# Kernel optimization log

Measured on AMD Instinct MI355X. Metric: run time of the kernel, lower is better.

Reference implementation:

```python
import jax, jax.numpy as jnp
import numpy as np

B, S, D_MODEL, D_QK = 4, 4096, 256, 64


def setup_inputs() -> dict:
    key = jax.random.key(0)
    ks = jax.random.split(key, 6)
    enc_q = jax.random.normal(ks[0], (B, S, D_MODEL), dtype=jnp.float32)
    enc_k = jax.random.normal(ks[1], (B, S, D_MODEL), dtype=jnp.float32)
    enc_v = jax.random.normal(ks[2], (B, S, D_MODEL), dtype=jnp.float32)
    # torch nn.Linear weight layout: [out_features, in_features]
    Wq = jax.random.normal(ks[3], (D_QK, D_MODEL), dtype=jnp.float32) * (D_MODEL ** -0.5)
    Wk = jax.random.normal(ks[4], (D_QK, D_MODEL), dtype=jnp.float32) * (D_MODEL ** -0.5)
    Wv = jax.random.normal(ks[5], (D_MODEL, D_MODEL), dtype=jnp.float32) * (D_MODEL ** -0.5)
    # causal mask: True above the diagonal -> masked out (matches masked_fill semantics)
    mask = jnp.triu(jnp.ones((S, S), dtype=jnp.bool_), k=1)
    return {"encodings_for_q": enc_q, "encodings_for_k": enc_k,
            "encodings_for_v": enc_v, "mask": mask,
            "Wq": Wq, "Wk": Wk, "Wv": Wv}


def reference(encodings_for_q, encodings_for_k, encodings_for_v, mask, Wq, Wk, Wv):
    # linear projections (no bias): x @ W.T
    q = jnp.einsum('bsd,qd->bsq', encodings_for_q, Wq)   # [B,S,d_qk]
    k = jnp.einsum('bsd,qd->bsq', encodings_for_k, Wk)   # [B,S,d_qk]
    v = jnp.einsum('bsd,ed->bse', encodings_for_v, Wv)   # [B,S,d_model]
    scale = k.shape[-1] ** 0.5                            # sqrt(d_qk)
    sims = jnp.einsum('bsq,btq->bst', q, k) / scale       # [B,S,S]
    sims = jnp.where(mask, jnp.float32(-1e9), sims)
    attn = jax.nn.softmax(sims, axis=-1)
    return jnp.einsum('bst,bte->bse', attn, v)            # [B,S,d_model]
```

## Files before the change

### kernel.cpp

```cpp
#include <hip/hip_runtime.h>


#define BATCH 4
#define SEQ   4096
#define DM    256
#define DQK   64

typedef __bf16 bf16x8 __attribute__((ext_vector_type(8)));
typedef __bf16 bf16x2 __attribute__((ext_vector_type(2)));
typedef float  f32x16 __attribute__((ext_vector_type(16)));

__device__ __forceinline__ unsigned short f2bf(float f) {
    __bf16 h = (__bf16)f;
    return __builtin_bit_cast(unsigned short, h);
}
__device__ __forceinline__ unsigned int pk2bf(float lo, float hi) {
    bf16x2 v = {(__bf16)lo, (__bf16)hi};
    return __builtin_bit_cast(unsigned int, v);
}
__device__ __forceinline__ bf16x8 u4bf(uint4 u) { return __builtin_bit_cast(bf16x8, u); }

__device__ __forceinline__ void repack_store(const f32x16& acc, int q2, int l,
                                             uint4* __restrict__ out, size_t tile_ofs_u4) {
    unsigned int d0[4], d1[4], p0[4], p1[4];
#pragma unroll
    for (int h = 0; h < 4; ++h) {
        d0[h] = pk2bf(acc[4*h + 0], acc[4*h + 1]);
        d1[h] = pk2bf(acc[4*h + 2], acc[4*h + 3]);
        p0[h] = __shfl_xor((int)d0[h], 32);
        p1[h] = __shfl_xor((int)d1[h], 32);
    }
#pragma unroll
    for (int kc = 0; kc < 2; ++kc) {
        int h = 2*kc + q2;
        uint4 v = (q2 == 0) ? make_uint4(d0[h], d1[h], p0[h], p1[h])
                            : make_uint4(p0[h], p1[h], d0[h], d1[h]);
        out[tile_ofs_u4 + (size_t)kc * 64 + l] = v;
    }
}

__device__ __forceinline__ int obase(int T) {
    return (T < 24) ? (T - 12) : 12 + (T - 24) * 2;
}
__device__ __forceinline__ int dbase(int T) {
    return (T < 24) ? (T - 12) * 2 : 24 + (T - 24) * 3;
}

__global__ __launch_bounds__(256) void proj(const float* __restrict__ Xq,
                                            const float* __restrict__ Xk,
                                            const float* __restrict__ Xv,
                                            const float* __restrict__ Wq,
                                            const float* __restrict__ Wk,
                                            const float* __restrict__ Wv,
                                            uint4* __restrict__ qf,
                                            uint4* __restrict__ kf,
                                            uint4* __restrict__ vf) {
    __shared__ unsigned short Xs[64][264];
    __shared__ unsigned short Ws[64][264];

    const int z = blockIdx.z;
    const int bx = blockIdx.x, b = blockIdx.y;
    const float* X = (z == 0) ? Xq : (z == 1) ? Xk : Xv;
    const float* W = (z == 0) ? Wq : (z == 1) ? Wk : Wv;
    const int s0 = bx * 64;
    const int tid = threadIdx.x, w = tid >> 6, l = tid & 63, ln = l & 31, q2 = l >> 5;

#pragma unroll
    for (int i = 0; i < 16; ++i) {
        int f = i * 256 + tid;
        int r = f >> 6, c4 = f & 63;
        float4 xv = *(const float4*)&X[((size_t)b * SEQ + s0 + r) * DM + c4 * 4];
        ushort4 h; h.x = f2bf(xv.x); h.y = f2bf(xv.y); h.z = f2bf(xv.z); h.w = f2bf(xv.w);
        *(ushort4*)&Xs[r][c4 * 4] = h;
    }

    if (z < 2) {
#pragma unroll
        for (int i = 0; i < 16; ++i) {
            int f = i * 256 + tid;
            int r = f >> 6, c4 = f & 63;
            float4 wv = *(const float4*)&W[(size_t)r * DM + c4 * 4];
            ushort4 h; h.x = f2bf(wv.x); h.y = f2bf(wv.y); h.z = f2bf(wv.z); h.w = f2bf(wv.w);
            *(ushort4*)&Ws[r][c4 * 4] = h;
        }
        __syncthreads();
        const int msub = w >> 1, nsub = w & 1;
        f32x16 a0 = {}, a1 = {};
#pragma unroll
        for (int c = 0; c < 16; c += 2) {
            bf16x8 af0 = u4bf(*(const uint4*)&Ws[msub*32 + ln][c*16 + q2*8]);
            bf16x8 bf0 = u4bf(*(const uint4*)&Xs[nsub*32 + ln][c*16 + q2*8]);
            a0 = __builtin_amdgcn_mfma_f32_32x32x16_bf16(af0, bf0, a0, 0, 0, 0);
            bf16x8 af1 = u4bf(*(const uint4*)&Ws[msub*32 + ln][(c+1)*16 + q2*8]);
            bf16x8 bf1 = u4bf(*(const uint4*)&Xs[nsub*32 + ln][(c+1)*16 + q2*8]);
            a1 = __builtin_amdgcn_mfma_f32_32x32x16_bf16(af1, bf1, a1, 0, 0, 0);
        }
        f32x16 acc = a0 + a1;
        size_t base = (((size_t)(b*128 + bx*2 + nsub)) * 4 + 2*msub) * 64;
        repack_store(acc, q2, l, (z == 0) ? qf : kf, base);
    } else {
        const int msub = w & 1, nsub = w >> 1;
        for (int ec = 0; ec < 4; ++ec) {
            __syncthreads();
#pragma unroll
            for (int i = 0; i < 16; ++i) {
                int f = i * 256 + tid;
                int r = f >> 6, c4 = f & 63;
                float4 wv = *(const float4*)&W[(size_t)(ec*64 + r) * DM + c4 * 4];
                ushort4 h; h.x = f2bf(wv.x); h.y = f2bf(wv.y); h.z = f2bf(wv.z); h.w = f2bf(wv.w);
                *(ushort4*)&Ws[r][c4 * 4] = h;
            }
            __syncthreads();
            f32x16 a0 = {}, a1 = {};
#pragma unroll
            for (int c = 0; c < 16; c += 2) {
                bf16x8 af0 = u4bf(*(const uint4*)&Xs[msub*32 + ln][c*16 + q2*8]);
                bf16x8 bf0 = u4bf(*(const uint4*)&Ws[nsub*32 + ln][c*16 + q2*8]);
                a0 = __builtin_amdgcn_mfma_f32_32x32x16_bf16(af0, bf0, a0, 0, 0, 0);
                bf16x8 af1 = u4bf(*(const uint4*)&Xs[msub*32 + ln][(c+1)*16 + q2*8]);
                bf16x8 bf1 = u4bf(*(const uint4*)&Ws[nsub*32 + ln][(c+1)*16 + q2*8]);
                a1 = __builtin_amdgcn_mfma_f32_32x32x16_bf16(af1, bf1, a1, 0, 0, 0);
            }
            f32x16 acc = a0 + a1;
            int et = ec*2 + nsub;
            size_t base = (((size_t)(b*8 + et)) * 256 + (size_t)bx*4 + msub*2) * 64;
            repack_store(acc, q2, l, vf, base);
        }
    }
}

__global__ __launch_bounds__(512, 2) void attn(const uint4* __restrict__ qf,
                                               const uint4* __restrict__ kf,
                                               const uint4* __restrict__ vf,
                                               float* __restrict__ out,
                                               unsigned short* __restrict__ Op,
                                               float* __restrict__ Dp) {
    __shared__ uint4 Pb[2][2][8][64];
    __shared__ float denp[4][2][64];
    __shared__ float dfin[64];

    const int bid = blockIdx.x;
    const int slot = bid & 7;
    const int b = slot >> 1, qh = slot & 1;
    const int task = bid >> 3;
    int T, cc, nc;
    if (task < 12)      { T = task;                cc = 0;               nc = 1; }
    else if (task < 36) { int q = task - 12; T = 12 + (q >> 1); cc = q & 1;       nc = 2; }
    else                { int q = task - 36; T = 24 + q / 3;    cc = q - 3*(q/3); nc = 3; }
    const int n = T + 1;
    const int j0 = cc * n / nc, j1 = (cc + 1) * n / nc;

    const int tid = threadIdx.x, w = tid >> 6, l = tid & 63, ln = l & 31, q2 = l >> 5;
    const int ks = w & 3, qg = w >> 2;
    const int qsub = qh * 2 + qg;
    const int et = w;
    const float cfac = 0.18033688011112042f;

    bf16x8 qv[4];
#pragma unroll
    for (int c = 0; c < 4; ++c)
        qv[c] = u4bf(qf[(((size_t)b*128 + T*4 + qsub) * 4 + c) * 64 + l]);

    f32x16 oa[2] = {};
    float den = 0.f;

    uint4 kaf[4];
#pragma unroll
    for (int c = 0; c < 4; ++c)
        kaf[c] = kf[(((size_t)b*128 + j0*4 + ks) * 4 + c) * 64 + l];

    for (int jt = j0; jt < j1; ++jt) {
        const int buf = jt & 1;
        const bool diag = (jt == T);

        uint4 vbs[8];
#pragma unroll
        for (int kc = 0; kc < 8; ++kc)
            vbs[kc] = vf[(((size_t)b*8 + et) * 256 + (size_t)jt*8 + kc) * 64 + l];

        f32x16 s = {};
#pragma unroll
        for (int c = 0; c < 4; ++c)
            s = __builtin_amdgcn_mfma_f32_32x32x16_bf16(u4bf(kaf[c]), qv[c], s, 0, 0, 0);

        float pv[16], pd = 0.f;
#pragma unroll
        for (int r = 0; r < 16; ++r) {
            float e = __builtin_exp2f(s[r] * cfac);
            if (diag) {
                int klocal = 4*q2 + (r & 3) + 8*(r >> 2);
                if (ks*32 + klocal > qsub*32 + ln) e = 0.f;
            }
            pv[r] = e; pd += e;
        }
        den += pd;
#pragma unroll
        for (int quad = 0; quad < 4; ++quad) {
            unsigned int lo = pk2bf(pv[4*quad + 0], pv[4*quad + 1]);
            unsigned int hi = pk2bf(pv[4*quad + 2], pv[4*quad + 3]);
            int kcg = ks*2 + (quad >> 1);
            int h   = quad & 1;
            char* dst = (char*)&Pb[buf][qg][kcg][h*32 + ln] + q2*8;
            *(uint2*)dst = make_uint2(lo, hi);
        }
        __syncthreads();
        if (jt + 1 < j1) {
#pragma unroll
            for (int c = 0; c < 4; ++c)
                kaf[c] = kf[(((size_t)b*128 + (jt+1)*4 + ks) * 4 + c) * 64 + l];
        }
#pragma unroll
        for (int kc = 0; kc < 8; ++kc) {
            bf16x8 vb = u4bf(vbs[kc]);
#pragma unroll
            for (int qsl = 0; qsl < 2; ++qsl) {
                bf16x8 pa = u4bf(Pb[buf][qsl][kc][l]);
                oa[qsl] = __builtin_amdgcn_mfma_f32_32x32x16_bf16(pa, vb, oa[qsl], 0, 0, 0);
            }
        }
    }

    denp[ks][qg][l] = den;
    __syncthreads();
    if (tid < 64) {
        int qgl = tid >> 5, qln = tid & 31;
        float sden = 0.f;
#pragma unroll
        for (int p = 0; p < 4; ++p)
#pragma unroll
            for (int hh = 0; hh < 2; ++hh)
                sden += denp[p][qgl][hh*32 + qln];
        dfin[tid] = (nc == 1) ? 1.0f / sden : sden;
    }
    __syncthreads();

    if (nc == 1) {
#pragma unroll
        for (int qsl = 0; qsl < 2; ++qsl)
#pragma unroll
            for (int r = 0; r < 16; ++r) {
                int qrow = qsl*32 + (r & 3) + 8*(r >> 2) + 4*q2;
                out[((size_t)b*SEQ + T*128 + qh*64 + qrow) * DM + et*32 + ln] = oa[qsl][r] * dfin[qrow];
            }
    } else if (cc == 0) {
#pragma unroll
        for (int qsl = 0; qsl < 2; ++qsl)
#pragma unroll
            for (int r = 0; r < 16; ++r) {
                int qrow = qsl*32 + (r & 3) + 8*(r >> 2) + 4*q2;
                out[((size_t)b*SEQ + T*128 + qh*64 + qrow) * DM + et*32 + ln] = oa[qsl][r];
            }
        if (tid < 64) Dp[((size_t)b*48 + dbase(T)) * 128 + qh*64 + tid] = dfin[tid];
    } else {
        size_t pidx = (size_t)b*28 + obase(T) + (cc - 1);
#pragma unroll
        for (int qsl = 0; qsl < 2; ++qsl)
#pragma unroll
            for (int r = 0; r < 16; ++r) {
                int qrow = qsl*32 + (r & 3) + 8*(r >> 2) + 4*q2;
                Op[(pidx*128 + qh*64 + qrow) * DM + et*32 + ln] = f2bf(oa[qsl][r]);
            }
        if (tid < 64) Dp[((size_t)b*48 + dbase(T) + cc) * 128 + qh*64 + tid] = dfin[tid];
    }
}

__global__ __launch_bounds__(256) void combine(const unsigned short* __restrict__ Op,
                                               const float* __restrict__ Dp,
                                               float* __restrict__ out) {
    const int T = 12 + blockIdx.x, b = blockIdx.y, qq = blockIdx.z;
    const int nc = (T < 24) ? 2 : 3;
    const int t = threadIdx.x;
    const size_t db = (size_t)b*48 + dbase(T);
    const size_t pb = (size_t)b*28 + obase(T);
#pragma unroll 4
    for (int r = 0; r < 32; ++r) {
        int q = qq*32 + r;
        size_t oofs = ((size_t)b*SEQ + T*128 + q) * DM + t;
        float sum = out[oofs];
        float dsum = 0.f;
        for (int c = 0; c < nc; ++c) dsum += Dp[(db + c)*128 + q];
        for (int c = 1; c < nc; ++c) {
            unsigned int uv = Op[((pb + c - 1)*128 + q) * DM + t];
            sum += __builtin_bit_cast(float, uv << 16);
        }
        out[oofs] = sum / dsum;
    }
}

extern "C" void kernel_launch(void* const* d_in, const int* in_sizes, int n_in,
                              void* d_out, int out_size, void* d_ws, size_t ws_size,
                              hipStream_t stream) {
    const float* enc_q = (const float*)d_in[0];
    const float* enc_k = (const float*)d_in[1];
    const float* enc_v = (const float*)d_in[2];
    const float* Wq = (const float*)d_in[4];
    const float* Wk = (const float*)d_in[5];
    const float* Wv = (const float*)d_in[6];
    float* out = (float*)d_out;

    uint4* qf = (uint4*)d_ws;
    uint4* kf = qf + 131072;
    uint4* vf = kf + 131072;
    unsigned short* Op = (unsigned short*)(vf + 524288);
    float* Dp = (float*)(Op + (size_t)4*28*128*256);

    proj<<<dim3(64, 4, 3), 256, 0, stream>>>(enc_q, enc_k, enc_v, Wq, Wk, Wv, qf, kf, vf);
    attn<<<480, 512, 0, stream>>>(qf, kf, vf, out, Op, Dp);
    combine<<<dim3(20, 4, 4), 256, 0, stream>>>(Op, Dp, out);
}
```

Measured before the change: 203.9 us.

## Split attention blocks over output halves, keep P in registers via lane shuffles

The attention kernel now launches twice as many 256-thread blocks, each handling half of the value/output columns, with every wave owning a 32-key slice for both query sub-tiles. P is passed to the PV MFMA through cross-lane shuffles instead of LDS, which removes the per-iteration __syncthreads. Partial outputs from the four key-slice waves are reduced through LDS at the end and written as vectorised stores. The trade is that QK^T and exp are recomputed by both output-half blocks, and the epilogue reduction adds extra LDS traffic and higher register pressure.

```diff
diff --git a/kernel.cpp b/kernel.cpp
--- a/kernel.cpp
+++ b/kernel.cpp
@@ -129,20 +129,21 @@
     }
 }
 
-__global__ __launch_bounds__(512, 2) void attn(const uint4* __restrict__ qf,
+__global__ __launch_bounds__(256, 2) void attn(const uint4* __restrict__ qf,
                                                const uint4* __restrict__ kf,
                                                const uint4* __restrict__ vf,
                                                float* __restrict__ out,
                                                unsigned short* __restrict__ Op,
                                                float* __restrict__ Dp) {
-    __shared__ uint4 Pb[2][2][8][64];
+    __shared__ float Lep[4][2][2][32][36];
     __shared__ float denp[4][2][64];
     __shared__ float dfin[64];
 
     const int bid = blockIdx.x;
     const int slot = bid & 7;
     const int b = slot >> 1, qh = slot & 1;
-    const int task = bid >> 3;
+    const int te = bid >> 3;
+    const int task = te >> 1, eh = te & 1;
     int T, cc, nc;
     if (task < 12)      { T = task;                cc = 0;               nc = 1; }
     else if (task < 36) { int q = task - 12; T = 12 + (q >> 1); cc = q & 1;       nc = 2; }
@@ -151,116 +152,152 @@
     const int j0 = cc * n / nc, j1 = (cc + 1) * n / nc;
 
     const int tid = threadIdx.x, w = tid >> 6, l = tid & 63, ln = l & 31, q2 = l >> 5;
-    const int ks = w & 3, qg = w >> 2;
-    const int qsub = qh * 2 + qg;
-    const int et = w;
+    const int ks = w;
     const float cfac = 0.18033688011112042f;
 
-    bf16x8 qv[4];
-#pragma unroll
-    for (int c = 0; c < 4; ++c)
-        qv[c] = u4bf(qf[(((size_t)b*128 + T*4 + qsub) * 4 + c) * 64 + l]);
-
-    f32x16 oa[2] = {};
-    float den = 0.f;
+    bf16x8 qv[2][4];
+#pragma unroll
+    for (int qs = 0; qs < 2; ++qs)
+#pragma unroll
+        for (int c = 0; c < 4; ++c)
+            qv[qs][c] = u4bf(qf[(((size_t)b*128 + T*4 + qh*2 + qs) * 4 + c) * 64 + l]);
 
     uint4 kaf[4];
 #pragma unroll
     for (int c = 0; c < 4; ++c)
         kaf[c] = kf[(((size_t)b*128 + j0*4 + ks) * 4 + c) * 64 + l];
 
+    f32x16 oa[2][4] = {};
+    float den[2] = {0.f, 0.f};
+
     for (int jt = j0; jt < j1; ++jt) {
-        const int buf = jt & 1;
         const bool diag = (jt == T);
 
-        uint4 vbs[8];
-#pragma unroll
-        for (int kc = 0; kc < 8; ++kc)
-            vbs[kc] = vf[(((size_t)b*8 + et) * 256 + (size_t)jt*8 + kc) * 64 + l];
-
-        f32x16 s = {};
-#pragma unroll
-        for (int c = 0; c < 4; ++c)
-            s = __builtin_amdgcn_mfma_f32_32x32x16_bf16(u4bf(kaf[c]), qv[c], s, 0, 0, 0);
-
-        float pv[16], pd = 0.f;
-#pragma unroll
-        for (int r = 0; r < 16; ++r) {
-            float e = __builtin_exp2f(s[r] * cfac);
-            if (diag) {
-                int klocal = 4*q2 + (r & 3) + 8*(r >> 2);
-                if (ks*32 + klocal > qsub*32 + ln) e = 0.f;
-            }
-            pv[r] = e; pd += e;
-        }
-        den += pd;
-#pragma unroll
-        for (int quad = 0; quad < 4; ++quad) {
-            unsigned int lo = pk2bf(pv[4*quad + 0], pv[4*quad + 1]);
-            unsigned int hi = pk2bf(pv[4*quad + 2], pv[4*quad + 3]);
-            int kcg = ks*2 + (quad >> 1);
-            int h   = quad & 1;
-            char* dst = (char*)&Pb[buf][qg][kcg][h*32 + ln] + q2*8;
-            *(uint2*)dst = make_uint2(lo, hi);
-        }
-        __syncthreads();
+        uint4 vbs[4][2];
+#pragma unroll
+        for (int e4 = 0; e4 < 4; ++e4)
+#pragma unroll
+            for (int t = 0; t < 2; ++t)
+                vbs[e4][t] = vf[(((size_t)b*8 + eh*4 + e4) * 256 + (size_t)jt*8 + ks*2 + t) * 64 + l];
+
+        f32x16 s0 = {}, s1 = {};
+#pragma unroll
+        for (int c = 0; c < 4; ++c) {
+            bf16x8 ka = u4bf(kaf[c]);
+            s0 = __builtin_amdgcn_mfma_f32_32x32x16_bf16(ka, qv[0][c], s0, 0, 0, 0);
+            s1 = __builtin_amdgcn_mfma_f32_32x32x16_bf16(ka, qv[1][c], s1, 0, 0, 0);
+        }
         if (jt + 1 < j1) {
 #pragma unroll
             for (int c = 0; c < 4; ++c)
                 kaf[c] = kf[(((size_t)b*128 + (jt+1)*4 + ks) * 4 + c) * 64 + l];
         }
-#pragma unroll
-        for (int kc = 0; kc < 8; ++kc) {
-            bf16x8 vb = u4bf(vbs[kc]);
-#pragma unroll
-            for (int qsl = 0; qsl < 2; ++qsl) {
-                bf16x8 pa = u4bf(Pb[buf][qsl][kc][l]);
-                oa[qsl] = __builtin_amdgcn_mfma_f32_32x32x16_bf16(pa, vb, oa[qsl], 0, 0, 0);
-            }
-        }
-    }
-
-    denp[ks][qg][l] = den;
+
+        uint4 pB[2][2];
+#pragma unroll
+        for (int qs = 0; qs < 2; ++qs) {
+            const f32x16 s = qs ? s1 : s0;
+            const int qsub = qh*2 + qs;
+            float pd = 0.f;
+            unsigned int own[8];
+#pragma unroll
+            for (int hq = 0; hq < 4; ++hq) {
+                float ev[4];
+#pragma unroll
+                for (int i = 0; i < 4; ++i) {
+                    float e = __builtin_exp2f(s[4*hq + i] * cfac);
+                    if (diag) {
+                        int klocal = 4*q2 + i + 8*hq;
+                        if (ks*32 + klocal > qsub*32 + ln) e = 0.f;
+                    }
+                    pd += e; ev[i] = e;
+                }
+                own[2*hq]     = pk2bf(ev[0], ev[1]);
+                own[2*hq + 1] = pk2bf(ev[2], ev[3]);
+            }
+            den[qs] += pd;
+            unsigned int xo[8];
+#pragma unroll
+            for (int i = 0; i < 8; ++i)
+                xo[i] = (unsigned int)__shfl_xor((int)own[i], 32);
+            pB[qs][0] = make_uint4(q2 ? xo[2] : own[0], q2 ? xo[3] : own[1],
+                                   q2 ? own[2] : xo[0], q2 ? own[3] : xo[1]);
+            pB[qs][1] = make_uint4(q2 ? xo[6] : own[4], q2 ? xo[7] : own[5],
+                                   q2 ? own[6] : xo[4], q2 ? own[7] : xo[5]);
+        }
+
+#pragma unroll
+        for (int e4 = 0; e4 < 4; ++e4) {
+            bf16x8 va0 = u4bf(vbs[e4][0]);
+            bf16x8 va1 = u4bf(vbs[e4][1]);
+#pragma unroll
+            for (int qs = 0; qs < 2; ++qs) {
+                oa[qs][e4] = __builtin_amdgcn_mfma_f32_32x32x16_bf16(va0, u4bf(pB[qs][0]), oa[qs][e4], 0, 0, 0);
+                oa[qs][e4] = __builtin_amdgcn_mfma_f32_32x32x16_bf16(va1, u4bf(pB[qs][1]), oa[qs][e4], 0, 0, 0);
+            }
+        }
+    }
+
+    denp[ks][0][l] = den[0];
+    denp[ks][1][l] = den[1];
     __syncthreads();
     if (tid < 64) {
-        int qgl = tid >> 5, qln = tid & 31;
+        int qsl = tid >> 5, qln = tid & 31;
         float sden = 0.f;
 #pragma unroll
         for (int p = 0; p < 4; ++p)
 #pragma unroll
             for (int hh = 0; hh < 2; ++hh)
-                sden += denp[p][qgl][hh*32 + qln];
+                sden += denp[p][qsl][hh*32 + qln];
         dfin[tid] = (nc == 1) ? 1.0f / sden : sden;
     }
     __syncthreads();
-
-    if (nc == 1) {
-#pragma unroll
-        for (int qsl = 0; qsl < 2; ++qsl)
-#pragma unroll
-            for (int r = 0; r < 16; ++r) {
-                int qrow = qsl*32 + (r & 3) + 8*(r >> 2) + 4*q2;
-                out[((size_t)b*SEQ + T*128 + qh*64 + qrow) * DM + et*32 + ln] = oa[qsl][r] * dfin[qrow];
-            }
-    } else if (cc == 0) {
-#pragma unroll
-        for (int qsl = 0; qsl < 2; ++qsl)
-#pragma unroll
-            for (int r = 0; r < 16; ++r) {
-                int qrow = qsl*32 + (r & 3) + 8*(r >> 2) + 4*q2;
-                out[((size_t)b*SEQ + T*128 + qh*64 + qrow) * DM + et*32 + ln] = oa[qsl][r];
-            }
-        if (tid < 64) Dp[((size_t)b*48 + dbase(T)) * 128 + qh*64 + tid] = dfin[tid];
-    } else {
-        size_t pidx = (size_t)b*28 + obase(T) + (cc - 1);
-#pragma unroll
-        for (int qsl = 0; qsl < 2; ++qsl)
-#pragma unroll
-            for (int r = 0; r < 16; ++r) {
-                int qrow = qsl*32 + (r & 3) + 8*(r >> 2) + 4*q2;
-                Op[(pidx*128 + qh*64 + qrow) * DM + et*32 + ln] = f2bf(oa[qsl][r]);
-            }
-        if (tid < 64) Dp[((size_t)b*48 + dbase(T) + cc) * 128 + qh*64 + tid] = dfin[tid];
+    if (eh == 0 && nc > 1 && tid < 64)
+        Dp[((size_t)b*48 + dbase(T) + cc) * 128 + qh*64 + tid] = dfin[tid];
+
+    const int qr  = (tid >> 3) & 31;
+    const int e4r = tid & 7;
+#pragma unroll
+    for (int ph = 0; ph < 2; ++ph) {
+#pragma unroll
+        for (int qs = 0; qs < 2; ++qs)
+#pragma unroll
+            for (int eti = 0; eti < 2; ++eti) {
+                const f32x16 a = oa[qs][ph*2 + eti];
+#pragma unroll
+                for (int h = 0; h < 4; ++h) {
+                    float4 v4 = make_float4(a[4*h], a[4*h+1], a[4*h+2], a[4*h+3]);
+                    *(float4*)&Lep[ks][qs][eti][ln][8*h + 4*q2] = v4;
+                }
+            }
+        __syncthreads();
+#pragma unroll
+        for (int qs = 0; qs < 2; ++qs)
+#pragma unroll
+            for (int eti = 0; eti < 2; ++eti) {
+                float4 sum = make_float4(0.f, 0.f, 0.f, 0.f);
+#pragma unroll
+                for (int p = 0; p < 4; ++p) {
+                    float4 v = *(const float4*)&Lep[p][qs][eti][qr][4*e4r];
+                    sum.x += v.x; sum.y += v.y; sum.z += v.z; sum.w += v.w;
+                }
+                const int qrow = qh*64 + qs*32 + qr;
+                const int eg   = eh*128 + (ph*2 + eti)*32 + 4*e4r;
+                if (nc == 1) {
+                    float d = dfin[qs*32 + qr];
+                    float4 o = make_float4(sum.x*d, sum.y*d, sum.z*d, sum.w*d);
+                    *(float4*)&out[((size_t)b*SEQ + T*128 + qrow) * DM + eg] = o;
+                } else if (cc == 0) {
+                    *(float4*)&out[((size_t)b*SEQ + T*128 + qrow) * DM + eg] = sum;
+                } else {
+                    size_t pidx = (size_t)b*28 + obase(T) + (cc - 1);
+                    uint2 u;
+                    u.x = pk2bf(sum.x, sum.y);
+                    u.y = pk2bf(sum.z, sum.w);
+                    *(uint2*)&Op[(pidx*128 + qrow) * DM + eg] = u;
+                }
+            }
+        if (ph == 0) __syncthreads();
     }
 }
 
@@ -305,6 +342,6 @@
     float* Dp = (float*)(Op + (size_t)4*28*128*256);
 
     proj<<<dim3(64, 4, 3), 256, 0, stream>>>(enc_q, enc_k, enc_v, Wq, Wk, Wv, qf, kf, vf);
-    attn<<<480, 512, 0, stream>>>(qf, kf, vf, out, Op, Dp);
+    attn<<<960, 256, 0, stream>>>(qf, kf, vf, out, Op, Dp);
     combine<<<dim3(20, 4, 4), 256, 0, stream>>>(Op, Dp, out);
 }
```

Result: slower. 224.3 us (+10.0%).

## Stream-K split of causal attention cells with atomic accumulation and normalize pass

Applied to the files above, without the earlier changes.

Replaces the fixed per-tile chunk split with a stream-K scheme: the 528 causal (query tile, key tile) cells per batch are divided evenly across 60 blocks. Each block walks its contiguous cell range and flushes partial outputs and denominators with atomicAdd into the zeroed output and a denominator buffer. A separate norm kernel then divides by the denominators, replacing the bf16 partial buffer and the combine kernel. This aims to balance load across blocks. The cost is two memsets, heavy float atomics on the full output, and nondeterministic summation order.

```diff
diff --git a/kernel.cpp b/kernel.cpp
--- a/kernel.cpp
+++ b/kernel.cpp
@@ -5,6 +5,7 @@
 #define SEQ   4096
 #define DM    256
 #define DQK   64
+#define NCELL 528
 
 typedef __bf16 bf16x8 __attribute__((ext_vector_type(8)));
 typedef __bf16 bf16x2 __attribute__((ext_vector_type(2)));
@@ -37,13 +38,6 @@
                             : make_uint4(p0[h], p1[h], d0[h], d1[h]);
         out[tile_ofs_u4 + (size_t)kc * 64 + l] = v;
     }
-}
-
-__device__ __forceinline__ int obase(int T) {
-    return (T < 24) ? (T - 12) : 12 + (T - 24) * 2;
-}
-__device__ __forceinline__ int dbase(int T) {
-    return (T < 24) ? (T - 12) * 2 : 24 + (T - 24) * 3;
 }
 
 __global__ __launch_bounds__(256) void proj(const float* __restrict__ Xq,
@@ -133,55 +127,53 @@
                                                const uint4* __restrict__ kf,
                                                const uint4* __restrict__ vf,
                                                float* __restrict__ out,
-                                               unsigned short* __restrict__ Op,
-                                               float* __restrict__ Dp) {
+                                               float* __restrict__ Den) {
     __shared__ uint4 Pb[2][2][8][64];
-    __shared__ float denp[4][2][64];
-    __shared__ float dfin[64];
 
     const int bid = blockIdx.x;
     const int slot = bid & 7;
     const int b = slot >> 1, qh = slot & 1;
-    const int task = bid >> 3;
-    int T, cc, nc;
-    if (task < 12)      { T = task;                cc = 0;               nc = 1; }
-    else if (task < 36) { int q = task - 12; T = 12 + (q >> 1); cc = q & 1;       nc = 2; }
-    else                { int q = task - 36; T = 24 + q / 3;    cc = q - 3*(q/3); nc = 3; }
-    const int n = T + 1;
-    const int j0 = cc * n / nc, j1 = (cc + 1) * n / nc;
+    const int blk = bid >> 3;
+    const int c0 = (blk * NCELL) / 60;
+    const int c1 = ((blk + 1) * NCELL) / 60;
+
+    int T = 0;
+    while ((T + 1) * (T + 2) / 2 <= c0) ++T;
+    int j = c0 - T * (T + 1) / 2;
 
     const int tid = threadIdx.x, w = tid >> 6, l = tid & 63, ln = l & 31, q2 = l >> 5;
     const int ks = w & 3, qg = w >> 2;
-    const int qsub = qh * 2 + qg;
     const int et = w;
     const float cfac = 0.18033688011112042f;
 
     bf16x8 qv[4];
 #pragma unroll
     for (int c = 0; c < 4; ++c)
-        qv[c] = u4bf(qf[(((size_t)b*128 + T*4 + qsub) * 4 + c) * 64 + l]);
+        qv[c] = u4bf(qf[(((size_t)b*128 + T*4 + qh*2 + qg) * 4 + c) * 64 + l]);
+
+    uint4 kaf[4];
+#pragma unroll
+    for (int c = 0; c < 4; ++c)
+        kaf[c] = kf[(((size_t)b*128 + j*4 + ks) * 4 + c) * 64 + l];
 
     f32x16 oa[2] = {};
     float den = 0.f;
-
-    uint4 kaf[4];
-#pragma unroll
-    for (int c = 0; c < 4; ++c)
-        kaf[c] = kf[(((size_t)b*128 + j0*4 + ks) * 4 + c) * 64 + l];
-
-    for (int jt = j0; jt < j1; ++jt) {
-        const int buf = jt & 1;
-        const bool diag = (jt == T);
+    bool dirty = false;
+
+    for (int c = c0; c < c1; ++c) {
+        const int buf = c & 1;
+        const bool diag = (j == T);
+        const int qsub = qh*2 + qg;
 
         uint4 vbs[8];
 #pragma unroll
         for (int kc = 0; kc < 8; ++kc)
-            vbs[kc] = vf[(((size_t)b*8 + et) * 256 + (size_t)jt*8 + kc) * 64 + l];
+            vbs[kc] = vf[(((size_t)b*8 + et) * 256 + (size_t)j*8 + kc) * 64 + l];
 
         f32x16 s = {};
 #pragma unroll
-        for (int c = 0; c < 4; ++c)
-            s = __builtin_amdgcn_mfma_f32_32x32x16_bf16(u4bf(kaf[c]), qv[c], s, 0, 0, 0);
+        for (int cc = 0; cc < 4; ++cc)
+            s = __builtin_amdgcn_mfma_f32_32x32x16_bf16(u4bf(kaf[cc]), qv[cc], s, 0, 0, 0);
 
         float pv[16], pd = 0.f;
 #pragma unroll
@@ -204,11 +196,16 @@
             *(uint2*)dst = make_uint2(lo, hi);
         }
         __syncthreads();
-        if (jt + 1 < j1) {
-#pragma unroll
-            for (int c = 0; c < 4; ++c)
-                kaf[c] = kf[(((size_t)b*128 + (jt+1)*4 + ks) * 4 + c) * 64 + l];
-        }
+
+        const bool endT = (j == T);
+        const int nT = endT ? T + 1 : T;
+        const int nj = endT ? 0 : j + 1;
+        if (c + 1 < c1) {
+#pragma unroll
+            for (int cc = 0; cc < 4; ++cc)
+                kaf[cc] = kf[(((size_t)b*128 + nj*4 + ks) * 4 + cc) * 64 + l];
+        }
+
 #pragma unroll
         for (int kc = 0; kc < 8; ++kc) {
             bf16x8 vb = u4bf(vbs[kc]);
@@ -218,72 +215,57 @@
                 oa[qsl] = __builtin_amdgcn_mfma_f32_32x32x16_bf16(pa, vb, oa[qsl], 0, 0, 0);
             }
         }
-    }
-
-    denp[ks][qg][l] = den;
-    __syncthreads();
-    if (tid < 64) {
-        int qgl = tid >> 5, qln = tid & 31;
-        float sden = 0.f;
-#pragma unroll
-        for (int p = 0; p < 4; ++p)
-#pragma unroll
-            for (int hh = 0; hh < 2; ++hh)
-                sden += denp[p][qgl][hh*32 + qln];
-        dfin[tid] = (nc == 1) ? 1.0f / sden : sden;
-    }
-    __syncthreads();
-
-    if (nc == 1) {
+        dirty = true;
+
+        if (endT) {
+            atomicAdd(&Den[(size_t)b*SEQ + T*128 + qh*64 + qg*32 + ln], den);
+#pragma unroll
+            for (int qsl = 0; qsl < 2; ++qsl)
+#pragma unroll
+                for (int r = 0; r < 16; ++r) {
+                    int qrow = qsl*32 + (r & 3) + 8*(r >> 2) + 4*q2;
+                    atomicAdd(&out[((size_t)b*SEQ + T*128 + qh*64 + qrow) * DM + et*32 + ln],
+                              oa[qsl][r]);
+                }
+            den = 0.f;
+            oa[0] = (f32x16){}; oa[1] = (f32x16){};
+            dirty = false;
+            if (c + 1 < c1) {
+#pragma unroll
+                for (int cc = 0; cc < 4; ++cc)
+                    qv[cc] = u4bf(qf[(((size_t)b*128 + nT*4 + qh*2 + qg) * 4 + cc) * 64 + l]);
+            }
+        }
+        T = nT; j = nj;
+    }
+
+    if (dirty) {
+        atomicAdd(&Den[(size_t)b*SEQ + T*128 + qh*64 + qg*32 + ln], den);
 #pragma unroll
         for (int qsl = 0; qsl < 2; ++qsl)
 #pragma unroll
             for (int r = 0; r < 16; ++r) {
                 int qrow = qsl*32 + (r & 3) + 8*(r >> 2) + 4*q2;
-                out[((size_t)b*SEQ + T*128 + qh*64 + qrow) * DM + et*32 + ln] = oa[qsl][r] * dfin[qrow];
-            }
-    } else if (cc == 0) {
-#pragma unroll
-        for (int qsl = 0; qsl < 2; ++qsl)
-#pragma unroll
-            for (int r = 0; r < 16; ++r) {
-                int qrow = qsl*32 + (r & 3) + 8*(r >> 2) + 4*q2;
-                out[((size_t)b*SEQ + T*128 + qh*64 + qrow) * DM + et*32 + ln] = oa[qsl][r];
-            }
-        if (tid < 64) Dp[((size_t)b*48 + dbase(T)) * 128 + qh*64 + tid] = dfin[tid];
-    } else {
-        size_t pidx = (size_t)b*28 + obase(T) + (cc - 1);
-#pragma unroll
-        for (int qsl = 0; qsl < 2; ++qsl)
-#pragma unroll
-            for (int r = 0; r < 16; ++r) {
-                int qrow = qsl*32 + (r & 3) + 8*(r >> 2) + 4*q2;
-                Op[(pidx*128 + qh*64 + qrow) * DM + et*32 + ln] = f2bf(oa[qsl][r]);
-            }
-        if (tid < 64) Dp[((size_t)b*48 + dbase(T) + cc) * 128 + qh*64 + tid] = dfin[tid];
-    }
-}
-
-__global__ __launch_bounds__(256) void combine(const unsigned short* __restrict__ Op,
-                                               const float* __restrict__ Dp,
-                                               float* __restrict__ out) {
-    const int T = 12 + blockIdx.x, b = blockIdx.y, qq = blockIdx.z;
-    const int nc = (T < 24) ? 2 : 3;
-    const int t = threadIdx.x;
-    const size_t db = (size_t)b*48 + dbase(T);
-    const size_t pb = (size_t)b*28 + obase(T);
-#pragma unroll 4
-    for (int r = 0; r < 32; ++r) {
-        int q = qq*32 + r;
-        size_t oofs = ((size_t)b*SEQ + T*128 + q) * DM + t;
-        float sum = out[oofs];
-        float dsum = 0.f;
-        for (int c = 0; c < nc; ++c) dsum += Dp[(db + c)*128 + q];
-        for (int c = 1; c < nc; ++c) {
-            unsigned int uv = Op[((pb + c - 1)*128 + q) * DM + t];
-            sum += __builtin_bit_cast(float, uv << 16);
-        }
-        out[oofs] = sum / dsum;
+                atomicAdd(&out[((size_t)b*SEQ + T*128 + qh*64 + qrow) * DM + et*32 + ln],
+                          oa[qsl][r]);
+            }
+    }
+}
+
+__global__ __launch_bounds__(256) void norm(float* __restrict__ out,
+                                            const float* __restrict__ Den) {
+    const int b = blockIdx.y;
+    const int r0 = blockIdx.x * 16;
+    const int tid = threadIdx.x;
+    float4* o4 = (float4*)(out + ((size_t)b*SEQ + r0) * DM);
+#pragma unroll
+    for (int i = 0; i < 4; ++i) {
+        int idx = i * 256 + tid;
+        int r = idx >> 6;
+        float d = Den[(size_t)b*SEQ + r0 + r];
+        float4 v = o4[idx];
+        v.x /= d; v.y /= d; v.z /= d; v.w /= d;
+        o4[idx] = v;
     }
 }
 
@@ -301,10 +283,11 @@
     uint4* qf = (uint4*)d_ws;
     uint4* kf = qf + 131072;
     uint4* vf = kf + 131072;
-    unsigned short* Op = (unsigned short*)(vf + 524288);
-    float* Dp = (float*)(Op + (size_t)4*28*128*256);
-
+    float* Den = (float*)(vf + 524288);
+
+    hipMemsetAsync(out, 0, (size_t)BATCH * SEQ * DM * sizeof(float), stream);
+    hipMemsetAsync(Den, 0, (size_t)BATCH * SEQ * sizeof(float), stream);
     proj<<<dim3(64, 4, 3), 256, 0, stream>>>(enc_q, enc_k, enc_v, Wq, Wk, Wv, qf, kf, vf);
-    attn<<<480, 512, 0, stream>>>(qf, kf, vf, out, Op, Dp);
-    combine<<<dim3(20, 4, 4), 256, 0, stream>>>(Op, Dp, out);
-}
+    attn<<<480, 512, 0, stream>>>(qf, kf, vf, out, Den);
+    norm<<<dim3(256, 4), 256, 0, stream>>>(out, Den);
+}
```

Result: slower. 212.2 us (+4.1%).
